# Optimization experiments

Measured on AMD Instinct MI355X. Metric: run time of the kernel, lower is better.

## Reference

```python
import jax, jax.numpy as jnp
import numpy as np

HIDDEN = 2048
HEADS = 16
HEAD = HIDDEN // HEADS  # 128
MB = 16                 # TTT mini-batch size
LR = 1.0                # inner (test-time) learning rate
ROPE_BASE = 10000.0
LN_EPS = 1e-5


def setup_inputs() -> dict:
    key = jax.random.key(0)
    ks = jax.random.split(key, 7)
    B, S = 4, 2048
    scale = HIDDEN ** -0.5
    x = jax.random.normal(ks[0], (B, S, HIDDEN), jnp.float32)
    Wk = jax.random.normal(ks[1], (HIDDEN, HIDDEN), jnp.float32) * scale
    Wv = jax.random.normal(ks[2], (HIDDEN, HIDDEN), jnp.float32) * scale
    Wo = jax.random.normal(ks[3], (HIDDEN, HIDDEN), jnp.float32) * scale
    ln_g = jnp.ones((HIDDEN,), jnp.float32)
    ln_b = jnp.zeros((HIDDEN,), jnp.float32)
    # initial TTT hidden-state weights, per (batch, head)
    W0 = jax.random.normal(ks[4], (B, HEADS, HEAD, HEAD), jnp.float32) * 0.02
    return {"x": x, "Wk": Wk, "Wv": Wv, "Wo": Wo, "ln_g": ln_g, "ln_b": ln_b, "W0": W0}


def _rotate_half(u):
    u1, u2 = jnp.split(u, 2, axis=-1)
    return jnp.concatenate([-u2, u1], axis=-1)


def _rope(k, seq_len):
    # k: [B, H, S, D]
    inv_freq = 1.0 / (ROPE_BASE ** (jnp.arange(0, HEAD, 2, dtype=jnp.float32) / HEAD))
    t = jnp.arange(seq_len, dtype=jnp.float32)
    freqs = t[:, None] * inv_freq[None, :]          # [S, D/2]
    emb = jnp.concatenate([freqs, freqs], axis=-1)  # [S, D]
    cos, sin = jnp.cos(emb), jnp.sin(emb)
    return k * cos[None, None] + _rotate_half(k) * sin[None, None]


def reference(x, Wk, Wv, Wo, ln_g, ln_b, W0):
    B, S, _ = x.shape
    # projections (nn.Linear convention: y = x @ W.T), split into heads
    k = (x @ Wk.T).reshape(B, S, HEADS, HEAD).transpose(0, 2, 1, 3)  # [B,H,S,D]
    v = (x @ Wv.T).reshape(B, S, HEADS, HEAD).transpose(0, 2, 1, 3)
    k = _rope(k, S)

    nc = S // MB
    # [nc, B, H, MB, D]
    kc = k.reshape(B, HEADS, nc, MB, HEAD).transpose(2, 0, 1, 3, 4)
    vc = v.reshape(B, HEADS, nc, MB, HEAD).transpose(2, 0, 1, 3, 4)

    def step(W, kv):
        k_c, v_c = kv                                   # [B,H,MB,D]
        pred = jnp.einsum('bhmd,bhde->bhme', k_c, W)    # f(k; W) = k W
        err = pred - v_c
        # grad of mean-MSE over (MB*D) elements w.r.t. W: 2/(MB*D) * k^T err
        grad = (2.0 / (MB * HEAD)) * jnp.einsum('bhmd,bhme->bhde', k_c, err)
        W_new = W - LR * grad                           # inner SGD step
        out = jnp.einsum('bhmd,bhde->bhme', k_c, W_new) # output with updated weights
        return W_new, out

    W_final, outs = jax.lax.scan(step, W0, (kc, vc))    # outs: [nc,B,H,MB,D]
    o = outs.transpose(1, 2, 0, 3, 4).reshape(B, HEADS, S, HEAD)
    o = o.transpose(0, 2, 1, 3).reshape(B, S, HIDDEN)

    # LayerNorm + output projection + residual
    mu = o.mean(-1, keepdims=True)
    var = o.var(-1, keepdims=True)
    o = (o - mu) / jnp.sqrt(var + LN_EPS) * ln_g + ln_b
    return x + o @ Wo.T
```

## Files before the change

### kernel.cpp

```cpp
#include <hip/hip_runtime.h>
#include <cstdint>
#include <cstddef>

typedef __attribute__((ext_vector_type(4))) float    f32x4;
typedef __attribute__((ext_vector_type(8))) __bf16   bf16x8;
typedef __attribute__((ext_vector_type(4))) short    s16x4;
typedef __attribute__((ext_vector_type(4))) uint32_t u32x4;
typedef __attribute__((ext_vector_type(2))) uint32_t u32x2;

__device__ __forceinline__ float bf2f(uint16_t h) {
    uint32_t u = ((uint32_t)h) << 16;
    return __builtin_bit_cast(float, u);
}
__device__ __forceinline__ uint16_t f2bf(float f) {
    uint32_t u = __builtin_bit_cast(uint32_t, f);
    uint32_t r = (u + 0x7fffu + ((u >> 16) & 1u)) >> 16;
    return (uint16_t)r;
}
__device__ __forceinline__ uint16_t f2bf_fast(float f) {
    __bf16 h = (__bf16)f;
    return __builtin_bit_cast(uint16_t, h);
}

__device__ __forceinline__ f32x4 mfma32(bf16x8 a, bf16x8 b, f32x4 c) {
    return __builtin_amdgcn_mfma_f32_16x16x32_bf16(a, b, c, 0, 0, 0);
}
__device__ __forceinline__ f32x4 mfma16(s16x4 a, s16x4 b, f32x4 c) {
    return __builtin_amdgcn_mfma_f32_16x16x16bf16_1k(a, b, c, 0, 0, 0);
}

__device__ __forceinline__ void gload16(const void* g, void* l) {
    __builtin_amdgcn_global_load_lds(
        (const __attribute__((address_space(1))) uint32_t*)g,
        (__attribute__((address_space(3))) uint32_t*)l, 16, 0, 0);
}

__global__ __launch_bounds__(256) void cvt_bf16(
    const float* __restrict__ s, uint16_t* __restrict__ d, int n4)
{
    int i = blockIdx.x * 256 + threadIdx.x;
    const int stride = gridDim.x * 256;
    for (; i < n4; i += stride) {
        f32x4 v = ((const f32x4*)s)[i];
        u32x2 p;
        p[0] = (uint32_t)f2bf(v[0]) | ((uint32_t)f2bf(v[1]) << 16);
        p[1] = (uint32_t)f2bf(v[2]) | ((uint32_t)f2bf(v[3]) << 16);
        ((u32x2*)d)[i] = p;
    }
}

template <bool F32OUT>
__global__ __launch_bounds__(256) void gemm_bt(
    const uint16_t* __restrict__ A, const uint16_t* __restrict__ B,
    void* __restrict__ Cv, const float* __restrict__ R,
    int M, int N, int K)
{
    __shared__ __align__(16) uint16_t lA[128 * 32];
    __shared__ __align__(16) uint16_t lB[128 * 32];
    const int tid = threadIdx.x;
    const int wv = tid >> 6, ln = tid & 63;
    const int l15 = ln & 15, q = ln >> 4;
    const int m0 = blockIdx.y * 128, n0 = blockIdx.x * 128;
    const int wm = (wv >> 1) * 64, wn = (wv & 1) * 64;

    const uint16_t* ga = A + (size_t)(m0 + wv * 32 + (ln >> 2)) * K + (ln & 3) * 8;
    const uint16_t* gb = B + (size_t)(n0 + wv * 32 + (ln >> 2)) * K + (ln & 3) * 8;
    uint16_t* la = lA + (wv * 32) * 32;
    uint16_t* lb = lB + (wv * 32) * 32;

    f32x4 acc[4][4];
    for (int i = 0; i < 4; i++)
        for (int j = 0; j < 4; j++)
            acc[i][j] = (f32x4){0.f, 0.f, 0.f, 0.f};

    for (int kt = 0; kt < K; kt += 32) {
        gload16(ga + kt, la);
        gload16(ga + (size_t)16 * K + kt, la + 16 * 32);
        gload16(gb + kt, lb);
        gload16(gb + (size_t)16 * K + kt, lb + 16 * 32);
        __syncthreads();

        bf16x8 af[4], bfv[4];
        for (int mt = 0; mt < 4; mt++)
            af[mt] = __builtin_bit_cast(bf16x8,
                *(const u32x4*)(lA + (wm + mt * 16 + l15) * 32 + q * 8));
        for (int nt = 0; nt < 4; nt++)
            bfv[nt] = __builtin_bit_cast(bf16x8,
                *(const u32x4*)(lB + (wn + nt * 16 + l15) * 32 + q * 8));
        for (int mt = 0; mt < 4; mt++)
            for (int nt = 0; nt < 4; nt++)
                acc[mt][nt] = mfma32(af[mt], bfv[nt], acc[mt][nt]);
        __syncthreads();
    }

    for (int mt = 0; mt < 4; mt++)
        for (int nt = 0; nt < 4; nt++)
            for (int r = 0; r < 4; r++) {
                int row = m0 + wm + mt * 16 + q * 4 + r;
                int col = n0 + wn + nt * 16 + l15;
                size_t idx = (size_t)row * N + col;
                float v = acc[mt][nt][r];
                if (F32OUT) {
                    ((float*)Cv)[idx] = v + R[idx];
                } else {
                    ((uint16_t*)Cv)[idx] = f2bf(v);
                }
            }
}

__global__ __launch_bounds__(64) void repack(
    const uint16_t* __restrict__ kb, const uint16_t* __restrict__ vb,
    uint16_t* __restrict__ kp, uint16_t* __restrict__ kt,
    uint16_t* __restrict__ vt)
{
    const int g = blockIdx.x;
    const int c = g & 127, h = (g >> 7) & 15, b = g >> 11;
    const int ln = threadIdx.x;
    const int m = ln >> 2, cb = (ln & 3) * 32;
    const size_t tok = (size_t)b * 2048 + c * 16 + m;
    const int s = c * 16 + m;
    const uint16_t* krow = kb + tok * 2048 + h * 128;
    const uint16_t* vrow = vb + tok * 2048 + h * 128;

    u32x4 kraw[4], praw[4], vraw[4];
    for (int i = 0; i < 4; i++) {
        kraw[i] = *(const u32x4*)(krow + cb + 8 * i);
        praw[i] = *(const u32x4*)(krow + (cb ^ 64) + 8 * i);
        vraw[i] = *(const u32x4*)(vrow + cb + 8 * i);
    }
    const uint16_t* ku = (const uint16_t*)kraw;
    const uint16_t* pu = (const uint16_t*)praw;
    const uint16_t* vu = (const uint16_t*)vraw;

    uint16_t ko[32];
    for (int j = 0; j < 32; j++) {
        int col = cb + j;
        int p = col & 63;
        float invf = exp2f((float)p * (-13.287712379549449f / 64.0f));
        float a = (float)s * invf;
        float sn, cs;
        __sincosf(a, &sn, &cs);
        float u1 = bf2f(ku[j]), u2 = bf2f(pu[j]);
        float o = (col < 64) ? (u1 * cs - u2 * sn) : (u1 * cs + u2 * sn);
        ko[j] = f2bf(o);
    }

    uint16_t* kpg = kp + (size_t)g * 2048;
    uint16_t* ktg = kt + (size_t)g * 2048;
    uint16_t* vtg = vt + (size_t)g * 2048;
    for (int i = 0; i < 4; i++) {
        u32x4 pk;
        uint32_t* pw = (uint32_t*)&pk;
        for (int w = 0; w < 4; w++)
            pw[w] = (uint32_t)ko[8 * i + 2 * w] | ((uint32_t)ko[8 * i + 2 * w + 1] << 16);
        *(u32x4*)(kpg + m * 128 + cb + 8 * i) = pk;
    }
    for (int j = 0; j < 32; j++) {
        ktg[(cb + j) * 16 + m] = ko[j];
        vtg[(cb + j) * 16 + m] = vu[j];
    }
}

__global__ __launch_bounds__(64, 1) void ttt_scan(
    const uint16_t* __restrict__ kp, const uint16_t* __restrict__ kt,
    const uint16_t* __restrict__ vt, const float* __restrict__ W0,
    uint16_t* __restrict__ O)
{
    __shared__ __align__(16) uint16_t wbp[16 * 136];

    const int bid = blockIdx.x;
    const int g  = bid & 63;
    const int e0 = (bid >> 6) * 16;
    const int h = g & 15, b = g >> 4;
    const int ln = threadIdx.x;
    const int l15 = ln & 15, q = ln >> 4;

    f32x4 W[8];
    {
        const float* w0p = W0 + (size_t)g * 128 * 128;
        #pragma unroll
        for (int mt = 0; mt < 8; mt++)
            for (int r = 0; r < 4; r++)
                W[mt][r] = w0p[(size_t)(16 * mt + 4 * q + r) * 128 + e0 + l15];
    }
    #pragma unroll
    for (int mt = 0; mt < 8; mt++) {
        uint32_t p0 = (uint32_t)f2bf_fast(W[mt][0]) | ((uint32_t)f2bf_fast(W[mt][1]) << 16);
        uint32_t p1 = (uint32_t)f2bf_fast(W[mt][2]) | ((uint32_t)f2bf_fast(W[mt][3]) << 16);
        u32x2 pp; pp[0] = p0; pp[1] = p1;
        *(u32x2*)(wbp + l15 * 136 + 16 * mt + 4 * q) = pp;
    }

    const uint16_t* kpw = kp + (size_t)g * 128 * 2048;
    const uint16_t* ktw = kt + (size_t)g * 128 * 2048;
    const uint16_t* vtw = vt + (size_t)g * 128 * 2048;
    uint16_t*     obase = O  + (size_t)b * 2048 * 2048 + h * 128 + e0;

    auto loadset = [&](int c, u32x4* afr, u32x2* ktr, u32x2* vvr) {
        const uint16_t* kc = kpw + (size_t)c * 2048;
        const uint16_t* tc = ktw + (size_t)c * 2048;
        const uint16_t* vc = vtw + (size_t)c * 2048;
        #pragma unroll
        for (int ks = 0; ks < 4; ks++)
            afr[ks] = *(const u32x4*)(kc + l15 * 128 + ks * 32 + q * 8);
        #pragma unroll
        for (int mt = 0; mt < 8; mt++)
            ktr[mt] = *(const u32x2*)(tc + (16 * mt + l15) * 16 + 4 * q);
        vvr[0] = *(const u32x2*)(vc + (e0 + l15) * 16 + 4 * q);
    };

    auto step = [&](int c, const u32x4* afr, const u32x2* ktr, const u32x2* vvr) {
        const int s0 = c * 16;

        f32x4 accA = (f32x4){0.f, 0.f, 0.f, 0.f};
        f32x4 accB = (f32x4){0.f, 0.f, 0.f, 0.f};
        f32x4 gacA = (f32x4){0.f, 0.f, 0.f, 0.f};
        f32x4 gacB = (f32x4){0.f, 0.f, 0.f, 0.f};
        #pragma unroll
        for (int ks = 0; ks < 4; ks++) {
            bf16x8 a = __builtin_bit_cast(bf16x8, afr[ks]);
            bf16x8 bb = __builtin_bit_cast(bf16x8,
                *(const u32x4*)(wbp + l15 * 136 + ks * 32 + q * 8));
            if (ks & 1) { accB = mfma32(a, bb, accB); gacB = mfma32(a, a, gacB); }
            else        { accA = mfma32(a, bb, accA); gacA = mfma32(a, a, gacA); }
        }
        f32x4 acc, gacc;
        #pragma unroll
        for (int r = 0; r < 4; r++) { acc[r] = accA[r] + accB[r]; gacc[r] = gacA[r] + gacB[r]; }

        s16x4 vv = __builtin_bit_cast(s16x4, vvr[0]);
        s16x4 es, gf;
        #pragma unroll
        for (int r = 0; r < 4; r++) {
            es[r] = (short)f2bf_fast((bf2f((uint16_t)vv[r]) - acc[r]) * (1.0f / 1024.0f));
            gf[r] = (short)f2bf_fast(gacc[r]);
        }

        f32x4 o = mfma16(gf, es, acc);

        #pragma unroll
        for (int mt = 0; mt < 8; mt++) {
            s16x4 kf = __builtin_bit_cast(s16x4, ktr[mt]);
            W[mt] = mfma16(kf, es, W[mt]);
        }

        #pragma unroll
        for (int r = 0; r < 4; r++)
            obase[(size_t)(s0 + 4 * q + r) * 2048 + l15] = f2bf_fast(o[r]);

        #pragma unroll
        for (int mt = 0; mt < 8; mt++) {
            uint32_t p0 = (uint32_t)f2bf_fast(W[mt][0]) | ((uint32_t)f2bf_fast(W[mt][1]) << 16);
            uint32_t p1 = (uint32_t)f2bf_fast(W[mt][2]) | ((uint32_t)f2bf_fast(W[mt][3]) << 16);
            u32x2 pp; pp[0] = p0; pp[1] = p1;
            *(u32x2*)(wbp + l15 * 136 + 16 * mt + 4 * q) = pp;
        }
    };

    u32x4 afA[4], afB[4];
    u32x2 ktA[8], ktB[8];
    u32x2 vvA[1], vvB[1];
    loadset(0, afA, ktA, vvA);
    loadset(1, afB, ktB, vvB);

    for (int c = 0; c < 128; c += 2) {
        step(c, afA, ktA, vvA);
        if (c < 126) loadset(c + 2, afA, ktA, vvA);
        step(c + 1, afB, ktB, vvB);
        if (c < 126) loadset(c + 3, afB, ktB, vvB);
    }
}

__global__ __launch_bounds__(256) void ln_kernel(
    const uint16_t* __restrict__ X, const float* __restrict__ Gm,
    const float* __restrict__ Bt, uint16_t* __restrict__ Y)
{
    const int row = blockIdx.x, t = threadIdx.x;
    const uint16_t* xr = X + (size_t)row * 2048 + t * 8;
    u32x4 raw = *(const u32x4*)xr;
    const uint16_t* pr = (const uint16_t*)&raw;
    float v[8];
    float s = 0.f, s2 = 0.f;
    for (int i = 0; i < 8; i++) {
        v[i] = bf2f(pr[i]);
        s += v[i];
        s2 += v[i] * v[i];
    }
    for (int off = 32; off; off >>= 1) {
        s  += __shfl_down(s, off, 64);
        s2 += __shfl_down(s2, off, 64);
    }
    __shared__ float red[8];
    if ((t & 63) == 0) { red[(t >> 6) * 2] = s; red[(t >> 6) * 2 + 1] = s2; }
    __syncthreads();
    float ts  = red[0] + red[2] + red[4] + red[6];
    float ts2 = red[1] + red[3] + red[5] + red[7];
    float mu  = ts * (1.0f / 2048.0f);
    float var = ts2 * (1.0f / 2048.0f) - mu * mu;
    float inv = rsqrtf(var + 1e-5f);
    uint16_t outv[8];
    for (int i = 0; i < 8; i++) {
        float y = (v[i] - mu) * inv * Gm[t * 8 + i] + Bt[t * 8 + i];
        outv[i] = f2bf(y);
    }
    u32x4 ov;
    __builtin_memcpy(&ov, outv, 16);
    *(u32x4*)(Y + (size_t)row * 2048 + t * 8) = ov;
}

extern "C" void kernel_launch(void* const* d_in, const int* in_sizes, int n_in,
                              void* d_out, int out_size, void* d_ws, size_t ws_size,
                              hipStream_t stream)
{
    const float* x  = (const float*)d_in[0];
    const float* Wk = (const float*)d_in[1];
    const float* Wv = (const float*)d_in[2];
    const float* Wo = (const float*)d_in[3];
    const float* lg = (const float*)d_in[4];
    const float* lb = (const float*)d_in[5];
    const float* W0 = (const float*)d_in[6];
    float* out = (float*)d_out;

    const size_t NTOK = 8192, HID = 2048;
    uint16_t* xb   = (uint16_t*)d_ws;
    uint16_t* wbuf = xb + NTOK * HID;
    uint16_t* kb   = wbuf + HID * HID;
    uint16_t* vb   = kb + NTOK * HID;
    uint16_t* kt   = vb + NTOK * HID;
    uint16_t* vt   = kt + NTOK * HID;
    uint16_t* kp   = xb;
    uint16_t* ob   = (uint16_t*)d_out;
    uint16_t* lnb  = kb;

    dim3 grid(16, 64), blk(256);
    const int nX4 = (int)(NTOK * HID / 4), nW4 = (int)(HID * HID / 4);

    cvt_bf16<<<4096, 256, 0, stream>>>(x, xb, nX4);
    cvt_bf16<<<4096, 256, 0, stream>>>(Wk, wbuf, nW4);
    gemm_bt<false><<<grid, blk, 0, stream>>>(xb, wbuf, kb, nullptr, 8192, 2048, 2048);
    cvt_bf16<<<4096, 256, 0, stream>>>(Wv, wbuf, nW4);
    gemm_bt<false><<<grid, blk, 0, stream>>>(xb, wbuf, vb, nullptr, 8192, 2048, 2048);
    repack<<<8192, 64, 0, stream>>>(kb, vb, kp, kt, vt);
    ttt_scan<<<512, 64, 0, stream>>>(kp, kt, vt, W0, ob);
    ln_kernel<<<8192, 256, 0, stream>>>(ob, lg, lb, lnb);
    cvt_bf16<<<4096, 256, 0, stream>>>(Wo, wbuf, nW4);
    gemm_bt<true><<<grid, blk, 0, stream>>>(lnb, wbuf, out, x, 8192, 2048, 2048);
}
```

Before: 631.3 us.

## Replace 128x128 GEMM with double-buffered swizzled 256x256 tile kernel

The three projection GEMMs move to a new kernel with 256x256 output tiles, 512 threads, a K step of 64 and two LDS buffers, so the next tile's global-to-LDS load is issued while the current one is being multiplied. The LDS layout uses an XOR swizzle on the column chunk to cut bank conflicts on the fragment reads, and each wave now computes a 128x64 sub-tile. The aim is more data reuse per loaded byte and less time spent waiting on loads. In exchange it needs about 128KB of LDS per block and many more accumulator registers, and the grid shrinks to 256 blocks, roughly one per CU.

```diff
diff --git a/kernel.cpp b/kernel.cpp
--- a/kernel.cpp
+++ b/kernel.cpp
@@ -50,56 +50,102 @@
 }
 
 template <bool F32OUT>
-__global__ __launch_bounds__(256) void gemm_bt(
+__global__ __launch_bounds__(512, 2) void gemm256(
     const uint16_t* __restrict__ A, const uint16_t* __restrict__ B,
     void* __restrict__ Cv, const float* __restrict__ R,
     int M, int N, int K)
 {
-    __shared__ __align__(16) uint16_t lA[128 * 32];
-    __shared__ __align__(16) uint16_t lB[128 * 32];
+    __shared__ __align__(16) uint16_t lA[2][256 * 64];
+    __shared__ __align__(16) uint16_t lB[2][256 * 64];
+
     const int tid = threadIdx.x;
-    const int wv = tid >> 6, ln = tid & 63;
+    const int w = tid >> 6, ln = tid & 63;
     const int l15 = ln & 15, q = ln >> 4;
-    const int m0 = blockIdx.y * 128, n0 = blockIdx.x * 128;
-    const int wm = (wv >> 1) * 64, wn = (wv & 1) * 64;
-
-    const uint16_t* ga = A + (size_t)(m0 + wv * 32 + (ln >> 2)) * K + (ln & 3) * 8;
-    const uint16_t* gb = B + (size_t)(n0 + wv * 32 + (ln >> 2)) * K + (ln & 3) * 8;
-    uint16_t* la = lA + (wv * 32) * 32;
-    uint16_t* lb = lB + (wv * 32) * 32;
-
-    f32x4 acc[4][4];
-    for (int i = 0; i < 4; i++)
+    const int wm = w >> 2, wn = w & 3;
+    const int m0 = blockIdx.y * 256, n0 = blockIdx.x * 256;
+
+    const int srow = w * 32 + (ln >> 3);
+    const int scol = ((ln & 7) ^ (ln >> 3)) * 8;
+    const uint16_t* gA = A + (size_t)(m0 + srow) * K + scol;
+    const uint16_t* gB = B + (size_t)(n0 + srow) * K + scol;
+
+    f32x4 acc[8][4];
+    #pragma unroll
+    for (int i = 0; i < 8; i++)
         for (int j = 0; j < 4; j++)
             acc[i][j] = (f32x4){0.f, 0.f, 0.f, 0.f};
 
-    for (int kt = 0; kt < K; kt += 32) {
-        gload16(ga + kt, la);
-        gload16(ga + (size_t)16 * K + kt, la + 16 * 32);
-        gload16(gb + kt, lb);
-        gload16(gb + (size_t)16 * K + kt, lb + 16 * 32);
+    const int xs  = (l15 & 7) * 8;
+    const int aro = (wm * 128 + l15) * 64;
+    const int bro = (wn * 64 + l15) * 64;
+    const int k0o = (q * 8) ^ xs;
+    const int k1o = (32 + q * 8) ^ xs;
+
+    auto stage = [&](int t) {
+        const int s = t & 1;
+        const int kt = t * 64;
+        #pragma unroll
+        for (int i = 0; i < 4; i++)
+            gload16(gA + (size_t)(i * 8) * K + kt, lA[s] + (w * 32 + i * 8) * 64);
+        #pragma unroll
+        for (int i = 0; i < 4; i++)
+            gload16(gB + (size_t)(i * 8) * K + kt, lB[s] + (w * 32 + i * 8) * 64);
+    };
+
+    const int ntk = K >> 6;
+    stage(0);
+    __syncthreads();
+
+    for (int t = 0; t < ntk; ++t) {
+        const int s = t & 1;
+        if (t + 1 < ntk) stage(t + 1);
+
+        const uint16_t* As = lA[s];
+        const uint16_t* Bs = lB[s];
+
+        bf16x8 a0[8], b0[4];
+        #pragma unroll
+        for (int mt = 0; mt < 8; mt++)
+            a0[mt] = __builtin_bit_cast(bf16x8,
+                *(const u32x4*)(As + aro + mt * 1024 + k0o));
+        #pragma unroll
+        for (int nt2 = 0; nt2 < 4; nt2++)
+            b0[nt2] = __builtin_bit_cast(bf16x8,
+                *(const u32x4*)(Bs + bro + nt2 * 1024 + k0o));
+        #pragma unroll
+        for (int mt = 0; mt < 8; mt++)
+            #pragma unroll
+            for (int nt2 = 0; nt2 < 4; nt2++)
+                acc[mt][nt2] = mfma32(a0[mt], b0[nt2], acc[mt][nt2]);
+
+        bf16x8 a1[8], b1[4];
+        #pragma unroll
+        for (int mt = 0; mt < 8; mt++)
+            a1[mt] = __builtin_bit_cast(bf16x8,
+                *(const u32x4*)(As + aro + mt * 1024 + k1o));
+        #pragma unroll
+        for (int nt2 = 0; nt2 < 4; nt2++)
+            b1[nt2] = __builtin_bit_cast(bf16x8,
+                *(const u32x4*)(Bs + bro + nt2 * 1024 + k1o));
+        #pragma unroll
+        for (int mt = 0; mt < 8; mt++)
+            #pragma unroll
+            for (int nt2 = 0; nt2 < 4; nt2++)
+                acc[mt][nt2] = mfma32(a1[mt], b1[nt2], acc[mt][nt2]);
+
         __syncthreads();
-
-        bf16x8 af[4], bfv[4];
-        for (int mt = 0; mt < 4; mt++)
-            af[mt] = __builtin_bit_cast(bf16x8,
-                *(const u32x4*)(lA + (wm + mt * 16 + l15) * 32 + q * 8));
-        for (int nt = 0; nt < 4; nt++)
-            bfv[nt] = __builtin_bit_cast(bf16x8,
-                *(const u32x4*)(lB + (wn + nt * 16 + l15) * 32 + q * 8));
-        for (int mt = 0; mt < 4; mt++)
-            for (int nt = 0; nt < 4; nt++)
-                acc[mt][nt] = mfma32(af[mt], bfv[nt], acc[mt][nt]);
-        __syncthreads();
-    }
-
-    for (int mt = 0; mt < 4; mt++)
-        for (int nt = 0; nt < 4; nt++)
+    }
+
+    #pragma unroll
+    for (int mt = 0; mt < 8; mt++)
+        #pragma unroll
+        for (int nt2 = 0; nt2 < 4; nt2++)
+            #pragma unroll
             for (int r = 0; r < 4; r++) {
-                int row = m0 + wm + mt * 16 + q * 4 + r;
-                int col = n0 + wn + nt * 16 + l15;
+                int row = m0 + wm * 128 + mt * 16 + q * 4 + r;
+                int col = n0 + wn * 64 + nt2 * 16 + l15;
                 size_t idx = (size_t)row * N + col;
-                float v = acc[mt][nt][r];
+                float v = acc[mt][nt2][r];
                 if (F32OUT) {
                     ((float*)Cv)[idx] = v + R[idx];
                 } else {
@@ -332,17 +378,17 @@
     uint16_t* ob   = (uint16_t*)d_out;
     uint16_t* lnb  = kb;
 
-    dim3 grid(16, 64), blk(256);
+    dim3 grid(8, 32), blk(512);
     const int nX4 = (int)(NTOK * HID / 4), nW4 = (int)(HID * HID / 4);
 
     cvt_bf16<<<4096, 256, 0, stream>>>(x, xb, nX4);
     cvt_bf16<<<4096, 256, 0, stream>>>(Wk, wbuf, nW4);
-    gemm_bt<false><<<grid, blk, 0, stream>>>(xb, wbuf, kb, nullptr, 8192, 2048, 2048);
+    gemm256<false><<<grid, blk, 0, stream>>>(xb, wbuf, kb, nullptr, 8192, 2048, 2048);
     cvt_bf16<<<4096, 256, 0, stream>>>(Wv, wbuf, nW4);
-    gemm_bt<false><<<grid, blk, 0, stream>>>(xb, wbuf, vb, nullptr, 8192, 2048, 2048);
+    gemm256<false><<<grid, blk, 0, stream>>>(xb, wbuf, vb, nullptr, 8192, 2048, 2048);
     repack<<<8192, 64, 0, stream>>>(kb, vb, kp, kt, vt);
     ttt_scan<<<512, 64, 0, stream>>>(kp, kt, vt, W0, ob);
     ln_kernel<<<8192, 256, 0, stream>>>(ob, lg, lb, lnb);
     cvt_bf16<<<4096, 256, 0, stream>>>(Wo, wbuf, nW4);
-    gemm_bt<true><<<grid, blk, 0, stream>>>(lnb, wbuf, out, x, 8192, 2048, 2048);
-}
+    gemm256<true><<<grid, blk, 0, stream>>>(lnb, wbuf, out, x, 8192, 2048, 2048);
+}
```

Measured after the change: 538.6 us. 14.7% less time.
